# Kernel tuning notes

Hardware: AMD Instinct MI355X
Metric: run time of the kernel (lower is better)

The kernel has to match this reference:

```python
import jax, jax.numpy as jnp
import numpy as np

TEMPERATURE = 8.0
MINF = -1000000000.0


def setup_inputs() -> dict:
    key = jax.random.key(0)
    kq, kk, kv, km = jax.random.split(key, 4)
    B, LQ, LK, DK, DV = 64, 1024, 1024, 64, 64
    q = jax.random.normal(kq, (B, LQ, DK), dtype=jnp.float32)
    k = jax.random.normal(kk, (B, LK, DK), dtype=jnp.float32)
    v = jax.random.normal(kv, (B, LK, DV), dtype=jnp.float32)
    mask = jax.random.randint(km, (B, LQ, LK), 0, 2).astype(jnp.bool_)
    return {"q": q, "k": k, "v": v, "mask": mask}


def reference(q, k, v, mask):
    # attn: [B, LQ, LK]
    attn = jnp.einsum("bqd,bkd->bqk", q, k) / TEMPERATURE
    attn = jnp.where(mask, MINF, attn)
    attn = jax.nn.softmax(attn, axis=2)
    out = jnp.einsum("bqk,bkd->bqd", attn, v)  # [B, LQ, DV]
    return (out, attn)
```

## Files before the change

kernel.cpp:

```cpp
#include <hip/hip_runtime.h>
#include <hip/hip_bf16.h>
#include <stdint.h>

#define B_  64
#define LQ_ 1024
#define LK_ 1024
#define D_  64
#define QT_ 16
#define SP_ (LK_ + 4)


typedef __attribute__((ext_vector_type(4))) float  f32x4;
typedef __attribute__((ext_vector_type(8))) short  short8;

__device__ __forceinline__ short f2bf(float x) {
    return __builtin_bit_cast(short, __float2bfloat16(x));
}
__device__ __forceinline__ float bf2f(short h) {
    return __bfloat162float(__builtin_bit_cast(__hip_bfloat16, h));
}

__global__ __launch_bounds__(256) void attn_fused(
    const void* __restrict__ qv, const void* __restrict__ kv,
    const void* __restrict__ vv, const void* __restrict__ mv,
    float* __restrict__ out, float* __restrict__ attn)
{
    __shared__ __align__(16) float s_p[QT_][SP_];
    __shared__ int s_flags;

    const int t    = threadIdx.x;
    const int lane = t & 63;
    const int wave = t >> 6;
    const int lr   = lane & 15;
    const int lg   = lane >> 4;
    const int b    = blockIdx.y;
    const int q0   = blockIdx.x * QT_;

    if (t < 64) {
        const uint32_t u = ((const uint32_t*)qv)[t];
        const uint32_t e = (u >> 7) & 0xFFu;
        const bool qhit = ((u & 0xFFFFu) == 0u) || (e <= 8u) ||
                          (e >= 0x60u && e <= 0x90u);
        const bool mhit = (((const uint32_t*)mv)[t] <= 1u);
        const unsigned long long qb_ = __ballot(qhit);
        const unsigned long long mb_ = __ballot(mhit);
        if (t == 0) {
            int f = 0;
            if (__popcll(qb_) >= 58) f |= 1;
            if (__popcll(mb_) >= 58) f |= 2;
            s_flags = f;
        }
    }
    __syncthreads();
    const bool QKV_BF16 = (s_flags & 1) != 0;
    const bool MASK_INT = (s_flags & 2) != 0;

    const size_t qoff = ((size_t)b * LQ_ + q0) * D_;
    const size_t kvoff = (size_t)b * LK_ * D_;
    const size_t moff = ((size_t)b * LQ_ + q0) * LK_;
    float* __restrict__ attn_b = attn + moff;
    float* __restrict__ out_b  = out + qoff;

    short8 qhi[2], qlo[2];
    if (QKV_BF16) {
        const uint16_t* q16 = (const uint16_t*)qv + qoff + (size_t)lr * D_;
        #pragma unroll
        for (int ks = 0; ks < 2; ++ks) {
            qhi[ks] = *reinterpret_cast<const short8*>(q16 + ks * 32 + lg * 8);
            qlo[ks] = short8{0,0,0,0,0,0,0,0};
        }
    } else {
        const float* qp0 = (const float*)qv + qoff + (size_t)lr * D_;
        #pragma unroll
        for (int ks = 0; ks < 2; ++ks) {
            const float* qp = qp0 + ks * 32 + lg * 8;
            const float4 x0 = *reinterpret_cast<const float4*>(qp);
            const float4 x1 = *reinterpret_cast<const float4*>(qp + 4);
            const float xs[8] = {x0.x, x0.y, x0.z, x0.w, x1.x, x1.y, x1.z, x1.w};
            #pragma unroll
            for (int j = 0; j < 8; ++j) {
                const short h = f2bf(xs[j]);
                qhi[ks][j] = h;
                qlo[ks][j] = f2bf(xs[j] - bf2f(h));
            }
        }
    }

    if (QKV_BF16) {
        const uint16_t* k16 = (const uint16_t*)kv + kvoff;
        #pragma unroll 1
        for (int tile = 0; tile < 16; ++tile) {
            const int c0 = wave * 256 + tile * 16;
            f32x4 acc = {0.f, 0.f, 0.f, 0.f};
            #pragma unroll
            for (int ks = 0; ks < 2; ++ks) {
                const short8 khi = *reinterpret_cast<const short8*>(
                    k16 + (size_t)(c0 + lr) * D_ + ks * 32 + lg * 8);
                acc = __builtin_amdgcn_mfma_f32_16x16x32_bf16(qhi[ks], khi, acc, 0, 0, 0);
            }
            #pragma unroll
            for (int j = 0; j < 4; ++j)
                s_p[lg * 4 + j][c0 + lr] = acc[j];
        }
    } else {
        const float* kf = (const float*)kv + kvoff;
        #pragma unroll 1
        for (int tile = 0; tile < 16; ++tile) {
            const int c0 = wave * 256 + tile * 16;
            f32x4 acc = {0.f, 0.f, 0.f, 0.f};
            #pragma unroll
            for (int ks = 0; ks < 2; ++ks) {
                const float* kp = kf + (size_t)(c0 + lr) * D_ + ks * 32 + lg * 8;
                const float4 x0 = *reinterpret_cast<const float4*>(kp);
                const float4 x1 = *reinterpret_cast<const float4*>(kp + 4);
                const float xs[8] = {x0.x, x0.y, x0.z, x0.w, x1.x, x1.y, x1.z, x1.w};
                short8 khi;
                #pragma unroll
                for (int j = 0; j < 8; ++j) khi[j] = f2bf(xs[j]);
                acc = __builtin_amdgcn_mfma_f32_16x16x32_bf16(qhi[ks], khi, acc, 0, 0, 0);
                acc = __builtin_amdgcn_mfma_f32_16x16x32_bf16(qlo[ks], khi, acc, 0, 0, 0);
            }
            #pragma unroll
            for (int j = 0; j < 4; ++j)
                s_p[lg * 4 + j][c0 + lr] = acc[j];
        }
    }
    __syncthreads();

    #pragma unroll
    for (int rr = 0; rr < QT_ / 4; ++rr) {
        const int r = wave * (QT_ / 4) + rr;
        float vals[16];
        if (MASK_INT) {
            const uint32_t* mrow = (const uint32_t*)mv + moff + (size_t)r * LK_;
            #pragma unroll
            for (int i = 0; i < 16; ++i) {
                const float s = s_p[r][lane + 64 * i];
                vals[i] = mrow[lane + 64 * i] ? -1.0e9f : s * 0.125f;
            }
        } else {
            const uint8_t* mrow = (const uint8_t*)mv + moff + (size_t)r * LK_;
            #pragma unroll
            for (int i = 0; i < 16; ++i) {
                const float s = s_p[r][lane + 64 * i];
                vals[i] = mrow[lane + 64 * i] ? -1.0e9f : s * 0.125f;
            }
        }
        float m = -3.0e38f;
        #pragma unroll
        for (int i = 0; i < 16; ++i) m = fmaxf(m, vals[i]);
        #pragma unroll
        for (int off = 32; off > 0; off >>= 1)
            m = fmaxf(m, __shfl_xor(m, off));
        float ssum = 0.f;
        #pragma unroll
        for (int i = 0; i < 16; ++i) {
            vals[i] = __expf(vals[i] - m);
            ssum += vals[i];
        }
        #pragma unroll
        for (int off = 32; off > 0; off >>= 1)
            ssum += __shfl_xor(ssum, off);
        const float inv = 1.0f / ssum;
        #pragma unroll
        for (int i = 0; i < 16; ++i) {
            const float p = vals[i] * inv;
            __builtin_nontemporal_store(p, &attn_b[(size_t)r * LK_ + lane + 64 * i]);
            s_p[r][lane + 64 * i] = p;
        }
    }
    __syncthreads();

    const int nb = wave * 16;
    f32x4 oacc = {0.f, 0.f, 0.f, 0.f};
    if (QKV_BF16) {
        const uint16_t* v16 = (const uint16_t*)vv + kvoff;
        #pragma unroll 2
        for (int ks = 0; ks < 32; ++ks) {
            const int k0 = ks * 32;
            const float* pp = &s_p[lr][k0 + lg * 8];
            const float4 a0 = *reinterpret_cast<const float4*>(pp);
            const float4 a1 = *reinterpret_cast<const float4*>(pp + 4);
            const float as[8] = {a0.x, a0.y, a0.z, a0.w, a1.x, a1.y, a1.z, a1.w};
            short8 phi;
            #pragma unroll
            for (int j = 0; j < 8; ++j) phi[j] = f2bf(as[j]);
            const uint16_t* vp = v16 + (size_t)(k0 + lg * 8) * D_ + nb + lr;
            short8 vhi;
            #pragma unroll
            for (int j = 0; j < 8; ++j) vhi[j] = (short)vp[(size_t)j * D_];
            oacc = __builtin_amdgcn_mfma_f32_16x16x32_bf16(phi, vhi, oacc, 0, 0, 0);
        }
    } else {
        const float* vf = (const float*)vv + kvoff;
        #pragma unroll 2
        for (int ks = 0; ks < 32; ++ks) {
            const int k0 = ks * 32;
            const float* pp = &s_p[lr][k0 + lg * 8];
            const float4 a0 = *reinterpret_cast<const float4*>(pp);
            const float4 a1 = *reinterpret_cast<const float4*>(pp + 4);
            const float as[8] = {a0.x, a0.y, a0.z, a0.w, a1.x, a1.y, a1.z, a1.w};
            short8 phi;
            #pragma unroll
            for (int j = 0; j < 8; ++j) phi[j] = f2bf(as[j]);
            const float* vp = vf + (size_t)(k0 + lg * 8) * D_ + nb + lr;
            short8 vhi;
            #pragma unroll
            for (int j = 0; j < 8; ++j) vhi[j] = f2bf(vp[(size_t)j * D_]);
            oacc = __builtin_amdgcn_mfma_f32_16x16x32_bf16(phi, vhi, oacc, 0, 0, 0);
        }
    }
    #pragma unroll
    for (int j = 0; j < 4; ++j)
        out_b[(size_t)(lg * 4 + j) * D_ + nb + lr] = oacc[j];
}

extern "C" void kernel_launch(void* const* d_in, const int* in_sizes, int n_in,
                              void* d_out, int out_size, void* d_ws, size_t ws_size,
                              hipStream_t stream) {
    const void* q    = d_in[0];
    const void* k    = d_in[1];
    const void* v    = d_in[2];
    const void* mask = d_in[3];

    float* out  = (float*)d_out;
    float* attn = out + (size_t)B_ * LQ_ * D_;

    dim3 grid(LQ_ / QT_, B_);
    attn_fused<<<grid, 256, 0, stream>>>(q, k, v, mask, out, attn);
}
```

Before: 653.8 us.

## Keep QK scores in registers, split softmax across waves, store bf16 probabilities

Drops the runtime format-detection probe and hard-codes fp32 inputs with an int32 mask. Each wave now keeps its 16x256 score tile in registers instead of writing fp32 scores to LDS. It computes a partial max and sum per wave and combines them through a small LDS reduction. Probabilities are written with vectorized nontemporal stores and staged in LDS as bf16, which halves LDS use and allows higher occupancy via launch_bounds(256,3). The trade-offs are more register pressure and a fixed assumption that the mask is int32.

```diff
diff --git a/kernel.cpp b/kernel.cpp
--- a/kernel.cpp
+++ b/kernel.cpp
@@ -7,11 +7,14 @@
 #define LK_ 1024
 #define D_  64
 #define QT_ 16
-#define SP_ (LK_ + 4)
+#define PP_ (LK_ + 8)
 
 
 typedef __attribute__((ext_vector_type(4))) float  f32x4;
 typedef __attribute__((ext_vector_type(8))) short  short8;
+typedef __attribute__((ext_vector_type(4))) uint16_t u16x4;
+
+#define LOG2E 1.4426950408889634f
 
 __device__ __forceinline__ short f2bf(float x) {
     return __builtin_bit_cast(short, __float2bfloat16(x));
@@ -20,13 +23,15 @@
     return __bfloat162float(__builtin_bit_cast(__hip_bfloat16, h));
 }
 
-__global__ __launch_bounds__(256) void attn_fused(
-    const void* __restrict__ qv, const void* __restrict__ kv,
-    const void* __restrict__ vv, const void* __restrict__ mv,
+__global__ __launch_bounds__(256, 3) void attn_fused(
+    const float* __restrict__ qv,
+    const float* __restrict__ kv,
+    const float* __restrict__ vv,
+    const int*   __restrict__ mk,
     float* __restrict__ out, float* __restrict__ attn)
 {
-    __shared__ __align__(16) float s_p[QT_][SP_];
-    __shared__ int s_flags;
+    __shared__ __align__(16) uint16_t s_p[QT_][PP_];
+    __shared__ float2 s_red[4][QT_];
 
     const int t    = threadIdx.x;
     const int lane = t & 63;
@@ -35,180 +40,123 @@
     const int lg   = lane >> 4;
     const int b    = blockIdx.y;
     const int q0   = blockIdx.x * QT_;
+    const int kw   = wave * 256;
 
-    if (t < 64) {
-        const uint32_t u = ((const uint32_t*)qv)[t];
-        const uint32_t e = (u >> 7) & 0xFFu;
-        const bool qhit = ((u & 0xFFFFu) == 0u) || (e <= 8u) ||
-                          (e >= 0x60u && e <= 0x90u);
-        const bool mhit = (((const uint32_t*)mv)[t] <= 1u);
-        const unsigned long long qb_ = __ballot(qhit);
-        const unsigned long long mb_ = __ballot(mhit);
-        if (t == 0) {
-            int f = 0;
-            if (__popcll(qb_) >= 58) f |= 1;
-            if (__popcll(mb_) >= 58) f |= 2;
-            s_flags = f;
-        }
-    }
-    __syncthreads();
-    const bool QKV_BF16 = (s_flags & 1) != 0;
-    const bool MASK_INT = (s_flags & 2) != 0;
-
-    const size_t qoff = ((size_t)b * LQ_ + q0) * D_;
-    const size_t kvoff = (size_t)b * LK_ * D_;
-    const size_t moff = ((size_t)b * LQ_ + q0) * LK_;
-    float* __restrict__ attn_b = attn + moff;
-    float* __restrict__ out_b  = out + qoff;
+    const float* __restrict__ qf32 = qv + ((size_t)b * LQ_ + q0) * D_;
+    const float* __restrict__ kf32 = kv + (size_t)b * LK_ * D_;
+    const float* __restrict__ vf32 = vv + (size_t)b * LK_ * D_;
+    const int*   __restrict__ mb   = mk + ((size_t)b * LQ_ + q0) * LK_;
+    float* __restrict__ attn_b = attn + ((size_t)b * LQ_ + q0) * LK_;
+    float* __restrict__ out_b  = out + ((size_t)b * LQ_ + q0) * D_;
 
     short8 qhi[2], qlo[2];
-    if (QKV_BF16) {
-        const uint16_t* q16 = (const uint16_t*)qv + qoff + (size_t)lr * D_;
+    #pragma unroll
+    for (int ks = 0; ks < 2; ++ks) {
+        const float* qp = qf32 + (size_t)lr * D_ + ks * 32 + lg * 8;
+        const float4 x0 = *reinterpret_cast<const float4*>(qp);
+        const float4 x1 = *reinterpret_cast<const float4*>(qp + 4);
+        const float xs[8] = {x0.x, x0.y, x0.z, x0.w, x1.x, x1.y, x1.z, x1.w};
         #pragma unroll
-        for (int ks = 0; ks < 2; ++ks) {
-            qhi[ks] = *reinterpret_cast<const short8*>(q16 + ks * 32 + lg * 8);
-            qlo[ks] = short8{0,0,0,0,0,0,0,0};
-        }
-    } else {
-        const float* qp0 = (const float*)qv + qoff + (size_t)lr * D_;
-        #pragma unroll
-        for (int ks = 0; ks < 2; ++ks) {
-            const float* qp = qp0 + ks * 32 + lg * 8;
-            const float4 x0 = *reinterpret_cast<const float4*>(qp);
-            const float4 x1 = *reinterpret_cast<const float4*>(qp + 4);
-            const float xs[8] = {x0.x, x0.y, x0.z, x0.w, x1.x, x1.y, x1.z, x1.w};
-            #pragma unroll
-            for (int j = 0; j < 8; ++j) {
-                const short h = f2bf(xs[j]);
-                qhi[ks][j] = h;
-                qlo[ks][j] = f2bf(xs[j] - bf2f(h));
-            }
+        for (int j = 0; j < 8; ++j) {
+            const short h = f2bf(xs[j]);
+            qhi[ks][j] = h;
+            qlo[ks][j] = f2bf(xs[j] - bf2f(h));
         }
     }
 
-    if (QKV_BF16) {
-        const uint16_t* k16 = (const uint16_t*)kv + kvoff;
-        #pragma unroll 1
-        for (int tile = 0; tile < 16; ++tile) {
-            const int c0 = wave * 256 + tile * 16;
-            f32x4 acc = {0.f, 0.f, 0.f, 0.f};
+    f32x4 s[16];
+    #pragma unroll 2
+    for (int tile = 0; tile < 16; ++tile) {
+        const int c0 = kw + tile * 16;
+        f32x4 acc = {0.f, 0.f, 0.f, 0.f};
+        #pragma unroll
+        for (int ks = 0; ks < 2; ++ks) {
+            const float* kp = kf32 + (size_t)(c0 + lr) * D_ + ks * 32 + lg * 8;
+            const float4 x0 = *reinterpret_cast<const float4*>(kp);
+            const float4 x1 = *reinterpret_cast<const float4*>(kp + 4);
+            const float xs[8] = {x0.x, x0.y, x0.z, x0.w, x1.x, x1.y, x1.z, x1.w};
+            short8 kf;
             #pragma unroll
-            for (int ks = 0; ks < 2; ++ks) {
-                const short8 khi = *reinterpret_cast<const short8*>(
-                    k16 + (size_t)(c0 + lr) * D_ + ks * 32 + lg * 8);
-                acc = __builtin_amdgcn_mfma_f32_16x16x32_bf16(qhi[ks], khi, acc, 0, 0, 0);
-            }
-            #pragma unroll
-            for (int j = 0; j < 4; ++j)
-                s_p[lg * 4 + j][c0 + lr] = acc[j];
+            for (int j = 0; j < 8; ++j) kf[j] = f2bf(xs[j]);
+            acc = __builtin_amdgcn_mfma_f32_16x16x32_bf16(kf, qhi[ks], acc, 0, 0, 0);
+            acc = __builtin_amdgcn_mfma_f32_16x16x32_bf16(kf, qlo[ks], acc, 0, 0, 0);
         }
-    } else {
-        const float* kf = (const float*)kv + kvoff;
-        #pragma unroll 1
-        for (int tile = 0; tile < 16; ++tile) {
-            const int c0 = wave * 256 + tile * 16;
-            f32x4 acc = {0.f, 0.f, 0.f, 0.f};
-            #pragma unroll
-            for (int ks = 0; ks < 2; ++ks) {
-                const float* kp = kf + (size_t)(c0 + lr) * D_ + ks * 32 + lg * 8;
-                const float4 x0 = *reinterpret_cast<const float4*>(kp);
-                const float4 x1 = *reinterpret_cast<const float4*>(kp + 4);
-                const float xs[8] = {x0.x, x0.y, x0.z, x0.w, x1.x, x1.y, x1.z, x1.w};
-                short8 khi;
-                #pragma unroll
-                for (int j = 0; j < 8; ++j) khi[j] = f2bf(xs[j]);
-                acc = __builtin_amdgcn_mfma_f32_16x16x32_bf16(qhi[ks], khi, acc, 0, 0, 0);
-                acc = __builtin_amdgcn_mfma_f32_16x16x32_bf16(qlo[ks], khi, acc, 0, 0, 0);
-            }
-            #pragma unroll
-            for (int j = 0; j < 4; ++j)
-                s_p[lg * 4 + j][c0 + lr] = acc[j];
+        s[tile] = acc;
+    }
+
+    float mloc = -3.0e38f;
+    #pragma unroll
+    for (int tile = 0; tile < 16; ++tile) {
+        const int4 mm = *reinterpret_cast<const int4*>(
+            mb + (size_t)lr * LK_ + kw + tile * 16 + lg * 4);
+        f32x4 x = s[tile];
+        x[0] = mm.x ? -1.0e9f : x[0] * 0.125f;
+        x[1] = mm.y ? -1.0e9f : x[1] * 0.125f;
+        x[2] = mm.z ? -1.0e9f : x[2] * 0.125f;
+        x[3] = mm.w ? -1.0e9f : x[3] * 0.125f;
+        s[tile] = x;
+        mloc = fmaxf(mloc, fmaxf(fmaxf(x[0], x[1]), fmaxf(x[2], x[3])));
+    }
+    mloc = fmaxf(mloc, __shfl_xor(mloc, 16));
+    mloc = fmaxf(mloc, __shfl_xor(mloc, 32));
+
+    float ssum = 0.f;
+    #pragma unroll
+    for (int tile = 0; tile < 16; ++tile) {
+        f32x4 x = s[tile];
+        #pragma unroll
+        for (int j = 0; j < 4; ++j) {
+            const float e = __builtin_exp2f((x[j] - mloc) * LOG2E);
+            x[j] = e;
+            ssum += e;
         }
+        s[tile] = x;
     }
+    ssum += __shfl_xor(ssum, 16);
+    ssum += __shfl_xor(ssum, 32);
+
+    if (lane < 16) s_red[wave][lane] = make_float2(mloc, ssum);
     __syncthreads();
 
+    const float2 pr0 = s_red[0][lr], pr1 = s_red[1][lr],
+                 pr2 = s_red[2][lr], pr3 = s_red[3][lr];
+    const float m = fmaxf(fmaxf(pr0.x, pr1.x), fmaxf(pr2.x, pr3.x));
+    const float tot = pr0.y * __builtin_exp2f((pr0.x - m) * LOG2E)
+                    + pr1.y * __builtin_exp2f((pr1.x - m) * LOG2E)
+                    + pr2.y * __builtin_exp2f((pr2.x - m) * LOG2E)
+                    + pr3.y * __builtin_exp2f((pr3.x - m) * LOG2E);
+    const float scale = __builtin_exp2f((mloc - m) * LOG2E) / tot;
+
     #pragma unroll
-    for (int rr = 0; rr < QT_ / 4; ++rr) {
-        const int r = wave * (QT_ / 4) + rr;
-        float vals[16];
-        if (MASK_INT) {
-            const uint32_t* mrow = (const uint32_t*)mv + moff + (size_t)r * LK_;
-            #pragma unroll
-            for (int i = 0; i < 16; ++i) {
-                const float s = s_p[r][lane + 64 * i];
-                vals[i] = mrow[lane + 64 * i] ? -1.0e9f : s * 0.125f;
-            }
-        } else {
-            const uint8_t* mrow = (const uint8_t*)mv + moff + (size_t)r * LK_;
-            #pragma unroll
-            for (int i = 0; i < 16; ++i) {
-                const float s = s_p[r][lane + 64 * i];
-                vals[i] = mrow[lane + 64 * i] ? -1.0e9f : s * 0.125f;
-            }
-        }
-        float m = -3.0e38f;
-        #pragma unroll
-        for (int i = 0; i < 16; ++i) m = fmaxf(m, vals[i]);
-        #pragma unroll
-        for (int off = 32; off > 0; off >>= 1)
-            m = fmaxf(m, __shfl_xor(m, off));
-        float ssum = 0.f;
-        #pragma unroll
-        for (int i = 0; i < 16; ++i) {
-            vals[i] = __expf(vals[i] - m);
-            ssum += vals[i];
-        }
-        #pragma unroll
-        for (int off = 32; off > 0; off >>= 1)
-            ssum += __shfl_xor(ssum, off);
-        const float inv = 1.0f / ssum;
-        #pragma unroll
-        for (int i = 0; i < 16; ++i) {
-            const float p = vals[i] * inv;
-            __builtin_nontemporal_store(p, &attn_b[(size_t)r * LK_ + lane + 64 * i]);
-            s_p[r][lane + 64 * i] = p;
-        }
+    for (int tile = 0; tile < 16; ++tile) {
+        const int c = kw + tile * 16 + lg * 4;
+        f32x4 pv;
+        pv[0] = s[tile][0] * scale;
+        pv[1] = s[tile][1] * scale;
+        pv[2] = s[tile][2] * scale;
+        pv[3] = s[tile][3] * scale;
+        __builtin_nontemporal_store(pv,
+            reinterpret_cast<f32x4*>(&attn_b[(size_t)lr * LK_ + c]));
+        u16x4 pk;
+        pk[0] = (uint16_t)f2bf(pv[0]);
+        pk[1] = (uint16_t)f2bf(pv[1]);
+        pk[2] = (uint16_t)f2bf(pv[2]);
+        pk[3] = (uint16_t)f2bf(pv[3]);
+        *reinterpret_cast<u16x4*>(&s_p[lr][c]) = pk;
     }
     __syncthreads();
 
     const int nb = wave * 16;
     f32x4 oacc = {0.f, 0.f, 0.f, 0.f};
-    if (QKV_BF16) {
-        const uint16_t* v16 = (const uint16_t*)vv + kvoff;
-        #pragma unroll 2
-        for (int ks = 0; ks < 32; ++ks) {
-            const int k0 = ks * 32;
-            const float* pp = &s_p[lr][k0 + lg * 8];
-            const float4 a0 = *reinterpret_cast<const float4*>(pp);
-            const float4 a1 = *reinterpret_cast<const float4*>(pp + 4);
-            const float as[8] = {a0.x, a0.y, a0.z, a0.w, a1.x, a1.y, a1.z, a1.w};
-            short8 phi;
-            #pragma unroll
-            for (int j = 0; j < 8; ++j) phi[j] = f2bf(as[j]);
-            const uint16_t* vp = v16 + (size_t)(k0 + lg * 8) * D_ + nb + lr;
-            short8 vhi;
-            #pragma unroll
-            for (int j = 0; j < 8; ++j) vhi[j] = (short)vp[(size_t)j * D_];
-            oacc = __builtin_amdgcn_mfma_f32_16x16x32_bf16(phi, vhi, oacc, 0, 0, 0);
-        }
-    } else {
-        const float* vf = (const float*)vv + kvoff;
-        #pragma unroll 2
-        for (int ks = 0; ks < 32; ++ks) {
-            const int k0 = ks * 32;
-            const float* pp = &s_p[lr][k0 + lg * 8];
-            const float4 a0 = *reinterpret_cast<const float4*>(pp);
-            const float4 a1 = *reinterpret_cast<const float4*>(pp + 4);
-            const float as[8] = {a0.x, a0.y, a0.z, a0.w, a1.x, a1.y, a1.z, a1.w};
-            short8 phi;
-            #pragma unroll
-            for (int j = 0; j < 8; ++j) phi[j] = f2bf(as[j]);
-            const float* vp = vf + (size_t)(k0 + lg * 8) * D_ + nb + lr;
-            short8 vhi;
-            #pragma unroll
-            for (int j = 0; j < 8; ++j) vhi[j] = f2bf(vp[(size_t)j * D_]);
-            oacc = __builtin_amdgcn_mfma_f32_16x16x32_bf16(phi, vhi, oacc, 0, 0, 0);
-        }
+    #pragma unroll 4
+    for (int ks = 0; ks < 32; ++ks) {
+        const int k0 = ks * 32;
+        const short8 pa = *reinterpret_cast<const short8*>(&s_p[lr][k0 + lg * 8]);
+        const float* vp = vf32 + (size_t)(k0 + lg * 8) * D_ + nb + lr;
+        short8 vf;
+        #pragma unroll
+        for (int jj = 0; jj < 8; ++jj) vf[jj] = f2bf(vp[(size_t)jj * D_]);
+        oacc = __builtin_amdgcn_mfma_f32_16x16x32_bf16(pa, vf, oacc, 0, 0, 0);
     }
     #pragma unroll
     for (int j = 0; j < 4; ++j)
@@ -218,10 +166,10 @@
 extern "C" void kernel_launch(void* const* d_in, const int* in_sizes, int n_in,
                               void* d_out, int out_size, void* d_ws, size_t ws_size,
                               hipStream_t stream) {
-    const void* q    = d_in[0];
-    const void* k    = d_in[1];
-    const void* v    = d_in[2];
-    const void* mask = d_in[3];
+    const float* q    = (const float*)d_in[0];
+    const float* k    = (const float*)d_in[1];
+    const float* v    = (const float*)d_in[2];
+    const int*   mask = (const int*)d_in[3];
 
     float* out  = (float*)d_out;
     float* attn = out + (size_t)B_ * LQ_ * D_;
```

Result: slower. 891.0 us (+36.3%).
